# Optimization experiments

Measured on AMD Instinct MI355X. Metric: run time of the kernel, lower is better.

Reference implementation:

```python
import jax, jax.numpy as jnp
import numpy as np

ALPHA = 1.0  # self.a buffer (alpha=1.0 default)


def setup_inputs() -> dict:
    key = jax.random.key(0)
    k1, k2, k3 = jax.random.split(key, 3)
    B, S, DIN, DOUT = 4, 2048, 4096, 4096
    # activations and weights are int8 in [-127, 127)
    x = jax.random.randint(k1, (B, S, DIN), -127, 127, dtype=jnp.int8)
    weight = jax.random.randint(k2, (DOUT, DIN), -127, 127, dtype=jnp.int8)
    bias = jax.random.normal(k3, (1, DOUT), dtype=jnp.float32)
    return {"x": x, "weight": weight, "bias": bias}


def reference(x, weight, bias):
    # x: [B, S, DIN] int8; weight: [DOUT, DIN] int8; bias: [1, DOUT] fp32
    x_shape = x.shape
    x2 = x.reshape(-1, x_shape[-1])  # [B*S, DIN]
    y = jnp.matmul(x2, weight.T, preferred_element_type=jnp.int32)  # [B*S, DOUT] int32
    # epilogue: y + round(bias / alpha); int32 + fp32 promotes to fp32 (matches torch)
    y = y.astype(jnp.float32) + jnp.round(bias / ALPHA)
    return y.reshape(*x_shape[:-1], y.shape[-1])
```

## Files before the change

kernel.cpp:

```cpp
#include <hip/hip_runtime.h>
#include <stdint.h>
#include <math.h>


typedef int i32x4 __attribute__((ext_vector_type(4)));

static constexpr int Mdim = 8192;
static constexpr int Ndim = 4096;
static constexpr int Kdim = 4096;
static constexpr int BM = 256;
static constexpr int BN = 256;
static constexpr int BKb = 128;
static constexpr int NKT = Kdim / BKb;
static constexpr int BUF_BYTES = 65536;

typedef const __attribute__((address_space(1))) unsigned int gu32;
typedef __attribute__((address_space(3))) unsigned int lu32;

__device__ __forceinline__ void gload_lds16(const int8_t* g, char* l) {
    __builtin_amdgcn_global_load_lds((gu32*)g, (lu32*)l, 16, 0, 0);
}

#define LGKM0_FENCE()  do { asm volatile("s_waitcnt lgkmcnt(0)" ::: "memory"); \
                            __builtin_amdgcn_sched_barrier(0); } while (0)

__global__ void pack_i32_to_i8_both(const int* __restrict__ X32,
                                    const int* __restrict__ W32,
                                    unsigned int* __restrict__ Xp,
                                    unsigned int* __restrict__ Wp,
                                    int nX4, int nT4) {
    int idx = blockIdx.x * blockDim.x + threadIdx.x;
    int stride = gridDim.x * blockDim.x;
    for (int i = idx; i < nT4; i += stride) {
        const int* src; unsigned int* dst; int j;
        if (i < nX4) { src = X32; dst = Xp; j = i; }
        else         { src = W32; dst = Wp; j = i - nX4; }
        i32x4 v = ((const i32x4*)src)[j];
        unsigned int o = ((unsigned)v[0] & 0xffu)
                       | (((unsigned)v[1] & 0xffu) << 8)
                       | (((unsigned)v[2] & 0xffu) << 16)
                       | (((unsigned)v[3]) << 24);
        dst[j] = o;
    }
}

__global__ __launch_bounds__(512, 2) void w8a8_gemm_256(
    const int8_t* __restrict__ X, const int8_t* __restrict__ Wt,
    const float* __restrict__ bias, float* __restrict__ out)
{
    __shared__ char smem[2 * BUF_BYTES];

    const int tid = threadIdx.x;
    const int w   = tid >> 6;
    const int l   = tid & 63;
    const int fr  = l & 15;
    const int fk  = l >> 4;
    const int wm  = w >> 2;
    const int wn  = w & 3;

    const int bm = blockIdx.x * BM;
    const int bn = blockIdx.y * BN;

    const int8_t* gA = X  + (size_t)(bm + l) * Kdim + w * 16;
    const int8_t* gB = Wt + (size_t)(bn + l) * Kdim + w * 16;
    const int ldsAw = w * 2048 + l * 16;
    const int ldsBw = 32768 + w * 2048 + l * 16;

    auto stageA = [&](int t, int hm) {
        const int bufo = (t & 1) * BUF_BYTES;
        const size_t ko = (size_t)t * BKb;
#pragma unroll
        for (int s = 0; s < 2; ++s)
            gload_lds16(gA + (size_t)(hm * 128 + s * 64) * Kdim + ko,
                        &smem[bufo + hm * 16384 + s * 1024 + ldsAw]);
    };
    auto stageB = [&](int t, int hn) {
        const int bufo = (t & 1) * BUF_BYTES;
        const size_t ko = (size_t)t * BKb;
#pragma unroll
        for (int s = 0; s < 2; ++s)
            gload_lds16(gB + (size_t)(hn * 128 + s * 64) * Kdim + ko,
                        &smem[bufo + hn * 16384 + s * 1024 + ldsBw]);
    };

    const int aBase = wm * 16384 + fk * 2048 + fr * 16;
    const int bBase = 32768 + (wn >> 1) * 16384 + fk * 2048
                    + ((wn & 1) * 64 + fr) * 16;

    i32x4 acc[8][4] = {};
    i32x4 a03[4][2], a47[4][2], b01[2][2], b23[2][2];

#define RD_A03(P) do { _Pragma("unroll") for (int ks = 0; ks < 2; ++ks) \
    _Pragma("unroll") for (int j = 0; j < 4; ++j) \
        a03[j][ks] = *(const i32x4*)&smem[(P) + aBase + ks * 8192 + j * 256]; } while (0)
#define RD_A47(P) do { _Pragma("unroll") for (int ks = 0; ks < 2; ++ks) \
    _Pragma("unroll") for (int j = 0; j < 4; ++j) \
        a47[j][ks] = *(const i32x4*)&smem[(P) + aBase + ks * 8192 + 1024 + j * 256]; } while (0)
#define RD_B01(P) do { _Pragma("unroll") for (int ks = 0; ks < 2; ++ks) \
    _Pragma("unroll") for (int ni = 0; ni < 2; ++ni) \
        b01[ni][ks] = *(const i32x4*)&smem[(P) + bBase + ks * 8192 + ni * 256]; } while (0)
#define RD_B23(P) do { _Pragma("unroll") for (int ks = 0; ks < 2; ++ks) \
    _Pragma("unroll") for (int ni = 0; ni < 2; ++ni) \
        b23[ni][ks] = *(const i32x4*)&smem[(P) + bBase + ks * 8192 + (2 + ni) * 256]; } while (0)

#define MFMA_Q(AF, BF, MO, NO) do { __builtin_amdgcn_s_setprio(1); \
    _Pragma("unroll") for (int ks = 0; ks < 2; ++ks) \
    _Pragma("unroll") for (int j = 0; j < 4; ++j) \
    _Pragma("unroll") for (int ni = 0; ni < 2; ++ni) \
        acc[(MO) + j][(NO) + ni] = __builtin_amdgcn_mfma_i32_16x16x64_i8( \
            AF[j][ks], BF[ni][ks], acc[(MO) + j][(NO) + ni], 0, 0, 0); \
    __builtin_amdgcn_s_setprio(0); } while (0)

    stageB(0, 0); stageB(0, 1); stageA(0, 0); stageA(0, 1);
    stageB(1, 0); stageB(1, 1);
    asm volatile("s_waitcnt vmcnt(4)" ::: "memory");
    __syncthreads();
    RD_A03(0); RD_B01(0);

#pragma unroll 1
    for (int t = 0; t < NKT; ++t) {
        const int p  = (t & 1) * BUF_BYTES;
        const int pn = ((t + 1) & 1) * BUF_BYTES;

        LGKM0_FENCE();
        RD_B23(p);
        if (t + 1 < NKT) stageA(t + 1, 0);
        __builtin_amdgcn_sched_barrier(0);
        MFMA_Q(a03, b01, 0, 0);

        LGKM0_FENCE();
        RD_A47(p);
        if (t + 1 < NKT) stageA(t + 1, 1);
        __builtin_amdgcn_sched_barrier(0);
        MFMA_Q(a03, b23, 0, 2);
        __builtin_amdgcn_s_barrier();

        LGKM0_FENCE();
        if (t + 2 < NKT) { stageB(t + 2, 0); stageB(t + 2, 1); }
        __builtin_amdgcn_sched_barrier(0);
        MFMA_Q(a47, b01, 4, 0);
        if (t + 2 < NKT)      asm volatile("s_waitcnt vmcnt(4)" ::: "memory");
        else if (t + 1 < NKT) asm volatile("s_waitcnt vmcnt(0)" ::: "memory");
        __builtin_amdgcn_s_barrier();

        if (t + 1 < NKT) { RD_A03(pn); RD_B01(pn); }
        __builtin_amdgcn_sched_barrier(0);
        MFMA_Q(a47, b23, 4, 2);
    }

    float bv[4];
#pragma unroll
    for (int ni = 0; ni < 4; ++ni)
        bv[ni] = rintf(bias[bn + wn * 64 + ni * 16 + fr]);
#pragma unroll
    for (int mi = 0; mi < 8; ++mi) {
        const int rbase = bm + wm * 128 + mi * 16 + fk * 4;
#pragma unroll
        for (int ni = 0; ni < 4; ++ni) {
            const int col = bn + wn * 64 + ni * 16 + fr;
#pragma unroll
            for (int r = 0; r < 4; ++r)
                out[(size_t)(rbase + r) * Ndim + col] = (float)acc[mi][ni][r] + bv[ni];
        }
    }
}

extern "C" void kernel_launch(void* const* d_in, const int* in_sizes, int n_in,
                              void* d_out, int out_size, void* d_ws, size_t ws_size,
                              hipStream_t stream) {
    const int*   X32  = (const int*)d_in[0];
    const int*   W32  = (const int*)d_in[1];
    const float* bias = (const float*)d_in[2];
    float* out = (float*)d_out;

    int8_t* Xp = (int8_t*)d_ws;
    int8_t* Wp = (int8_t*)d_ws + (size_t)Mdim * Kdim;

    const int nX4 = Mdim * Kdim / 4;
    const int nW4 = Ndim * Kdim / 4;
    pack_i32_to_i8_both<<<4096, 256, 0, stream>>>(
        X32, W32, (unsigned int*)Xp, (unsigned int*)Wp, nX4, nX4 + nW4);

    dim3 grid(Mdim / BM, Ndim / BN);
    w8a8_gemm_256<<<grid, dim3(512), 0, stream>>>(Xp, Wp, bias, out);
}
```

Before: 415.1 us.

## Switch to 32x32x32 int8 MFMA with new LDS layout and block swizzle

Replaces the 16x16x64 int8 MFMA tiles with 32x32x32 MFMA tiles. This changes the LDS staging layout, the fragment read patterns, the accumulator shape and the epilogue row mapping. It also remaps block indices so that groups of adjacent blocks share tiles, aiming for better L2 reuse. The larger MFMA issues fewer instructions and fewer LDS reads per FLOP, but the new LDS layout may cause bank conflicts and the epilogue stores are strided differently.

Measured after the change: 414.0 us. Within noise of the previous version (-0.2%).

```diff
diff --git a/kernel.cpp b/kernel.cpp
--- a/kernel.cpp
+++ b/kernel.cpp
@@ -4,6 +4,7 @@
 
 
 typedef int i32x4 __attribute__((ext_vector_type(4)));
+typedef int i32x16 __attribute__((ext_vector_type(16)));
 
 static constexpr int Mdim = 8192;
 static constexpr int Ndim = 4096;
@@ -50,72 +51,70 @@
 {
     __shared__ char smem[2 * BUF_BYTES];
 
-    const int tid = threadIdx.x;
-    const int w   = tid >> 6;
-    const int l   = tid & 63;
-    const int fr  = l & 15;
-    const int fk  = l >> 4;
-    const int wm  = w >> 2;
-    const int wn  = w & 3;
+    const int tid  = threadIdx.x;
+    const int w    = tid >> 6;
+    const int l    = tid & 63;
+    const int lrow = l & 31;
+    const int kh   = l >> 5;
+    const int wm   = w >> 2;
+    const int wn   = w & 3;
 
-    const int bm = blockIdx.x * BM;
-    const int bn = blockIdx.y * BN;
+    const int bid = blockIdx.y * gridDim.x + blockIdx.x;
+    const int swz = (bid & 7) * 64 + (bid >> 3);
+    const int bm  = (swz & 31) * BM;
+    const int bn  = (swz >> 5) * BN;
 
     const int8_t* gA = X  + (size_t)(bm + l) * Kdim + w * 16;
     const int8_t* gB = Wt + (size_t)(bn + l) * Kdim + w * 16;
-    const int ldsAw = w * 2048 + l * 16;
-    const int ldsBw = 32768 + w * 2048 + l * 16;
+    const int ldsAw = w * 4096 + l * 16;
+    const int ldsBw = 32768 + w * 4096 + l * 16;
 
-    auto stageA = [&](int t, int hm) {
+    auto stageA = [&](int t, int h) {
         const int bufo = (t & 1) * BUF_BYTES;
         const size_t ko = (size_t)t * BKb;
 #pragma unroll
-        for (int s = 0; s < 2; ++s)
-            gload_lds16(gA + (size_t)(hm * 128 + s * 64) * Kdim + ko,
-                        &smem[bufo + hm * 16384 + s * 1024 + ldsAw]);
+        for (int s = 2 * h; s < 2 * h + 2; ++s)
+            gload_lds16(gA + (size_t)(s * 64) * Kdim + ko,
+                        &smem[bufo + s * 1024 + ldsAw]);
     };
-    auto stageB = [&](int t, int hn) {
+    auto stageB = [&](int t, int h) {
         const int bufo = (t & 1) * BUF_BYTES;
         const size_t ko = (size_t)t * BKb;
 #pragma unroll
-        for (int s = 0; s < 2; ++s)
-            gload_lds16(gB + (size_t)(hn * 128 + s * 64) * Kdim + ko,
-                        &smem[bufo + hn * 16384 + s * 1024 + ldsBw]);
+        for (int s = 2 * h; s < 2 * h + 2; ++s)
+            gload_lds16(gB + (size_t)(s * 64) * Kdim + ko,
+                        &smem[bufo + s * 1024 + ldsBw]);
     };
 
-    const int aBase = wm * 16384 + fk * 2048 + fr * 16;
-    const int bBase = 32768 + (wn >> 1) * 16384 + fk * 2048
-                    + ((wn & 1) * 64 + fr) * 16;
+    const int aBase = kh * 4096 + wm * 2048 + lrow * 16;
+    const int bBase = 32768 + kh * 4096 + wn * 1024 + lrow * 16;
 
-    i32x4 acc[8][4] = {};
-    i32x4 a03[4][2], a47[4][2], b01[2][2], b23[2][2];
+    i32x16 acc[4][2] = {};
+    i32x4 a01[2][4], a23[2][4], b0[4], b1[4];
 
-#define RD_A03(P) do { _Pragma("unroll") for (int ks = 0; ks < 2; ++ks) \
-    _Pragma("unroll") for (int j = 0; j < 4; ++j) \
-        a03[j][ks] = *(const i32x4*)&smem[(P) + aBase + ks * 8192 + j * 256]; } while (0)
-#define RD_A47(P) do { _Pragma("unroll") for (int ks = 0; ks < 2; ++ks) \
-    _Pragma("unroll") for (int j = 0; j < 4; ++j) \
-        a47[j][ks] = *(const i32x4*)&smem[(P) + aBase + ks * 8192 + 1024 + j * 256]; } while (0)
-#define RD_B01(P) do { _Pragma("unroll") for (int ks = 0; ks < 2; ++ks) \
-    _Pragma("unroll") for (int ni = 0; ni < 2; ++ni) \
-        b01[ni][ks] = *(const i32x4*)&smem[(P) + bBase + ks * 8192 + ni * 256]; } while (0)
-#define RD_B23(P) do { _Pragma("unroll") for (int ks = 0; ks < 2; ++ks) \
-    _Pragma("unroll") for (int ni = 0; ni < 2; ++ni) \
-        b23[ni][ks] = *(const i32x4*)&smem[(P) + bBase + ks * 8192 + (2 + ni) * 256]; } while (0)
+#define RD_A01(P) do { _Pragma("unroll") for (int ki = 0; ki < 4; ++ki) \
+    _Pragma("unroll") for (int mi = 0; mi < 2; ++mi) \
+        a01[mi][ki] = *(const i32x4*)&smem[(P) + aBase + ki * 8192 + mi * 512]; } while (0)
+#define RD_A23(P) do { _Pragma("unroll") for (int ki = 0; ki < 4; ++ki) \
+    _Pragma("unroll") for (int mi = 0; mi < 2; ++mi) \
+        a23[mi][ki] = *(const i32x4*)&smem[(P) + aBase + ki * 8192 + (2 + mi) * 512]; } while (0)
+#define RD_B0(P) do { _Pragma("unroll") for (int ki = 0; ki < 4; ++ki) \
+        b0[ki] = *(const i32x4*)&smem[(P) + bBase + ki * 8192]; } while (0)
+#define RD_B1(P) do { _Pragma("unroll") for (int ki = 0; ki < 4; ++ki) \
+        b1[ki] = *(const i32x4*)&smem[(P) + bBase + ki * 8192 + 512]; } while (0)
 
 #define MFMA_Q(AF, BF, MO, NO) do { __builtin_amdgcn_s_setprio(1); \
-    _Pragma("unroll") for (int ks = 0; ks < 2; ++ks) \
-    _Pragma("unroll") for (int j = 0; j < 4; ++j) \
-    _Pragma("unroll") for (int ni = 0; ni < 2; ++ni) \
-        acc[(MO) + j][(NO) + ni] = __builtin_amdgcn_mfma_i32_16x16x64_i8( \
-            AF[j][ks], BF[ni][ks], acc[(MO) + j][(NO) + ni], 0, 0, 0); \
+    _Pragma("unroll") for (int ki = 0; ki < 4; ++ki) \
+    _Pragma("unroll") for (int mi = 0; mi < 2; ++mi) \
+        acc[(MO) + mi][NO] = __builtin_amdgcn_mfma_i32_32x32x32_i8( \
+            AF[mi][ki], BF[ki], acc[(MO) + mi][NO], 0, 0, 0); \
     __builtin_amdgcn_s_setprio(0); } while (0)
 
     stageB(0, 0); stageB(0, 1); stageA(0, 0); stageA(0, 1);
     stageB(1, 0); stageB(1, 1);
     asm volatile("s_waitcnt vmcnt(4)" ::: "memory");
     __syncthreads();
-    RD_A03(0); RD_B01(0);
+    RD_A01(0); RD_B0(0);
 
 #pragma unroll 1
     for (int t = 0; t < NKT; ++t) {
@@ -123,44 +122,46 @@
         const int pn = ((t + 1) & 1) * BUF_BYTES;
 
         LGKM0_FENCE();
-        RD_B23(p);
+        RD_B1(p);
         if (t + 1 < NKT) stageA(t + 1, 0);
         __builtin_amdgcn_sched_barrier(0);
-        MFMA_Q(a03, b01, 0, 0);
+        MFMA_Q(a01, b0, 0, 0);
 
         LGKM0_FENCE();
-        RD_A47(p);
+        RD_A23(p);
         if (t + 1 < NKT) stageA(t + 1, 1);
         __builtin_amdgcn_sched_barrier(0);
-        MFMA_Q(a03, b23, 0, 2);
+        MFMA_Q(a01, b1, 0, 1);
         __builtin_amdgcn_s_barrier();
 
         LGKM0_FENCE();
         if (t + 2 < NKT) { stageB(t + 2, 0); stageB(t + 2, 1); }
         __builtin_amdgcn_sched_barrier(0);
-        MFMA_Q(a47, b01, 4, 0);
+        MFMA_Q(a23, b0, 2, 0);
         if (t + 2 < NKT)      asm volatile("s_waitcnt vmcnt(4)" ::: "memory");
         else if (t + 1 < NKT) asm volatile("s_waitcnt vmcnt(0)" ::: "memory");
         __builtin_amdgcn_s_barrier();
 
-        if (t + 1 < NKT) { RD_A03(pn); RD_B01(pn); }
+        if (t + 1 < NKT) { RD_A01(pn); RD_B0(pn); }
         __builtin_amdgcn_sched_barrier(0);
-        MFMA_Q(a47, b23, 4, 2);
+        MFMA_Q(a23, b1, 2, 1);
     }
 
-    float bv[4];
+    float bv[2];
 #pragma unroll
-    for (int ni = 0; ni < 4; ++ni)
-        bv[ni] = rintf(bias[bn + wn * 64 + ni * 16 + fr]);
+    for (int ni = 0; ni < 2; ++ni)
+        bv[ni] = rintf(bias[bn + wn * 64 + ni * 32 + lrow]);
 #pragma unroll
-    for (int mi = 0; mi < 8; ++mi) {
-        const int rbase = bm + wm * 128 + mi * 16 + fk * 4;
+    for (int mi = 0; mi < 4; ++mi) {
+        const int rbase = bm + wm * 128 + mi * 32 + 4 * kh;
 #pragma unroll
-        for (int ni = 0; ni < 4; ++ni) {
-            const int col = bn + wn * 64 + ni * 16 + fr;
+        for (int ni = 0; ni < 2; ++ni) {
+            const int col = bn + wn * 64 + ni * 32 + lrow;
 #pragma unroll
-            for (int r = 0; r < 4; ++r)
-                out[(size_t)(rbase + r) * Ndim + col] = (float)acc[mi][ni][r] + bv[ni];
+            for (int r = 0; r < 16; ++r) {
+                const int row = rbase + (r & 3) + 8 * (r >> 2);
+                out[(size_t)row * Ndim + col] = (float)acc[mi][ni][r] + bv[ni];
+            }
         }
     }
 }
```
